# Performance work log

Hardware: AMD Instinct MI355X
Metric: run time of the kernel (lower is better)

## Reference

```python
import jax, jax.numpy as jnp
import numpy as np
import math

B, S, D, H, TD = 256, 200, 64, 512, 8


def setup_inputs():
    key = jax.random.key(0)
    ks = jax.random.split(key, 12)
    sd, sh, so = 1.0 / math.sqrt(D), 1.0 / math.sqrt(H), 1.0 / math.sqrt(H + TD)
    return dict(
        x=jax.random.normal(ks[0], (B, S, D), jnp.float32),
        a=jax.random.normal(ks[3], (B, TD), jnp.float32),
        t=jnp.cumsum(jax.random.uniform(ks[2], (B, S), jnp.float32), axis=1),
        mask=(jax.random.uniform(ks[1], (B, S, D)) < 0.8).astype(jnp.float32),
        w_dg_x=jax.random.normal(ks[4], (D,), jnp.float32) * sd,
        b_dg_x=jnp.zeros((D,), jnp.float32),
        W_dg_h=jax.random.normal(ks[5], (H, D), jnp.float32) * sd,
        b_dg_h=jnp.zeros((H,), jnp.float32),
        W=jax.random.normal(ks[6], (3 * H, D), jnp.float32) * sd,
        U=jax.random.normal(ks[7], (3 * H, H), jnp.float32) * sh,
        V=jax.random.normal(ks[8], (3 * H, D), jnp.float32) * sd,
        b=jnp.zeros((3 * H,), jnp.float32),
        attn_v=jnp.ones((H,), jnp.float32),
        W_out=jax.random.normal(ks[9], (H, H + TD), jnp.float32) * so,
        b_out=jnp.zeros((H,), jnp.float32),
    )


def reference(x, a, t, mask, w_dg_x, b_dg_x, W_dg_h, b_dg_h, W, U, V, b, attn_v, W_out, b_out):
    # ---- GRU-D preprocessing: per-feature time gaps delta ----
    x_tm = jnp.transpose(x, (1, 0, 2))    # (S,B,D) time-major
    m_tm = jnp.transpose(mask, (1, 0, 2))
    dt = jnp.diff(t, axis=1, prepend=t[:, :1])      # (B,S), dt[0]=0
    dt_tm = jnp.transpose(dt)[:, :, None]           # (S,B,1)
    # delta[i] = dt[i] + (1 - mask[i-1]) * delta[i-1]; ones at step 0 -> delta[0]=0
    m_prev = jnp.concatenate([jnp.ones((1,) + m_tm.shape[1:], m_tm.dtype), m_tm[:-1]], axis=0)

    def delta_step(d, inp):
        dt_i, mp_i = inp
        d = dt_i + (1.0 - mp_i) * d
        return d, d

    _, delta_tm = jax.lax.scan(delta_step, jnp.zeros((B, D), x.dtype), (dt_tm, m_prev))

    # empirical mean of observed values for imputation
    x_mean = (mask * x).sum((0, 1)) / jnp.maximum(mask.sum((0, 1)), 1.0)  # (D,)

    Wz, Wr, Wh = W[:H], W[H:2 * H], W[2 * H:]
    Uz, Ur, Uh = U[:H], U[H:2 * H], U[2 * H:]
    Vz, Vr, Vh = V[:H], V[H:2 * H], V[2 * H:]
    bz, br, bh = b[:H], b[H:2 * H], b[2 * H:]

    def cell(carry, inp):
        h, x_last = carry
        x_i, m_i, d_i = inp                                        # (B,D) each
        gamma_x = jnp.exp(-jax.nn.relu(w_dg_x * d_i + b_dg_x))     # (B,D) input decay
        gamma_h = jnp.exp(-jax.nn.relu(d_i @ W_dg_h.T + b_dg_h))   # (B,H) hidden decay
        x_hat = m_i * x_i + (1.0 - m_i) * (gamma_x * x_last + (1.0 - gamma_x) * x_mean)
        h_dec = gamma_h * h
        z = jax.nn.sigmoid(x_hat @ Wz.T + h_dec @ Uz.T + m_i @ Vz.T + bz)
        r = jax.nn.sigmoid(x_hat @ Wr.T + h_dec @ Ur.T + m_i @ Vr.T + br)
        h_til = jnp.tanh(x_hat @ Wh.T + (r * h_dec) @ Uh.T + m_i @ Vh.T + bh)
        h_new = (1.0 - z) * h_dec + z * h_til
        x_last_new = m_i * x_i + (1.0 - m_i) * x_last
        return (h_new, x_last_new), h_new

    init = (jnp.zeros((B, H), x.dtype), jnp.zeros((B, D), x.dtype))
    _, h_all = jax.lax.scan(cell, init, (x_tm, m_tm, delta_tm))    # (S,B,H)

    # ---- attention pooling over time (softmax along seq dim, as in torch dim=0) ----
    score = (h_all @ attn_v) / math.sqrt(H)        # (S,B)
    w_attn = jax.nn.softmax(score, axis=0)
    attn_h = (h_all * w_attn[..., None]).sum(0)    # (B,H)

    # ---- treatment head ----
    return jnp.concatenate([attn_h, a], axis=1) @ W_out.T + b_out  # (B,H)
```

## Files before the change

### kernel.cpp

```cpp
#include <hip/hip_runtime.h>
#include <hip/hip_bf16.h>
#include <stdint.h>


typedef unsigned short u16;
typedef unsigned int   u32;
typedef unsigned long long u64;
typedef short bfrag  __attribute__((ext_vector_type(8)));
typedef u16   u16x8  __attribute__((ext_vector_type(8)));
typedef float f32x4  __attribute__((ext_vector_type(4)));

#define NB 256
#define NS 200
#define ND 64
#define NH 512

union UQ  { u16x8 h; bfrag s; u64 u[2]; uint4 q; };
union UF2 { float f[2]; u64 u; };

__device__ __forceinline__ float b2f(u16 v){ union { float f; u32 u; } c; c.u = ((u32)v) << 16; return c.f; }
__device__ __forceinline__ u16 f2b(float f){ union { float f; u32 u; } c; c.f = f; u32 r = c.u + 0x7FFFu + ((c.u >> 16) & 1u); return (u16)(r >> 16); }
__device__ __forceinline__ float sigm(float x){ return 1.f / (1.f + __expf(-x)); }
__device__ __forceinline__ float tanh_f(float x){ return 1.f - 2.f / (1.f + __expf(2.f * x)); }

__device__ __forceinline__ u64 cload64(const void* p){
  return __hip_atomic_load((const u64*)p, __ATOMIC_RELAXED, __HIP_MEMORY_SCOPE_AGENT);
}
__device__ __forceinline__ void cstore64(void* p, u64 v){
  __hip_atomic_store((u64*)p, v, __ATOMIC_RELAXED, __HIP_MEMORY_SCOPE_AGENT);
}
__device__ __forceinline__ void load8f_c(const float* p, float* f){
  UF2 w;
  w.u = cload64(p + 0); f[0]=w.f[0]; f[1]=w.f[1];
  w.u = cload64(p + 2); f[2]=w.f[0]; f[3]=w.f[1];
  w.u = cload64(p + 4); f[4]=w.f[0]; f[5]=w.f[1];
  w.u = cload64(p + 6); f[6]=w.f[0]; f[7]=w.f[1];
}
__device__ __forceinline__ void store8f_c(float* p, const float* f){
  UF2 w;
  w.f[0]=f[0]; w.f[1]=f[1]; cstore64(p + 0, w.u);
  w.f[0]=f[2]; w.f[1]=f[3]; cstore64(p + 2, w.u);
  w.f[0]=f[4]; w.f[1]=f[5]; cstore64(p + 4, w.u);
  w.f[0]=f[6]; w.f[1]=f[7]; cstore64(p + 6, w.u);
}
__device__ __forceinline__ void spin_ge(u32* f, u32 tgt){
  while (__hip_atomic_load(f, __ATOMIC_RELAXED, __HIP_MEMORY_SCOPE_AGENT) < tgt)
    __builtin_amdgcn_s_sleep(2);
}
__device__ __forceinline__ bfrag ldfrag(const float* src){
  f32x4 lo = *(const f32x4*)src;
  f32x4 hi = *(const f32x4*)(src + 4);
  UQ z;
  z.h[0]=f2b(lo[0]); z.h[1]=f2b(lo[1]); z.h[2]=f2b(lo[2]); z.h[3]=f2b(lo[3]);
  z.h[4]=f2b(hi[0]); z.h[5]=f2b(hi[1]); z.h[6]=f2b(hi[2]); z.h[7]=f2b(hi[3]);
  return z.s;
}


__global__ void transpose_k(const float* __restrict__ Wout, float* __restrict__ WT){
  int i = blockIdx.x * 256 + threadIdx.x;
  if (i < 520 * 512) { int k = i >> 9, ho = i & 511; WT[i] = Wout[ho * 520 + k]; }
}

__global__ void mean1_k(const float* __restrict__ x, const float* __restrict__ mask,
                        float* __restrict__ PX, float* __restrict__ PM){
  int s = blockIdx.x, tid = threadIdx.x;
  __shared__ float lx[256], lm[256];
  float xa = 0.f, ma = 0.f;
  for (int i = tid; i < NB * ND; i += 256) {
    int b = i >> 6, d = i & 63;
    size_t ix = ((size_t)b * NS + s) * 64 + d;
    float m = mask[ix];
    xa += m * x[ix]; ma += m;
  }
  lx[tid] = xa; lm[tid] = ma;
  __syncthreads();
  if (tid < 64) {
    PX[(size_t)s * 64 + tid] = lx[tid] + lx[tid + 64] + lx[tid + 128] + lx[tid + 192];
    PM[(size_t)s * 64 + tid] = lm[tid] + lm[tid + 64] + lm[tid + 128] + lm[tid + 192];
  }
}

__global__ void mean2_k(const float* __restrict__ PX, const float* __restrict__ PM,
                        float* __restrict__ XMEAN){
  int d = threadIdx.x;
  float sx = 0.f, sm = 0.f;
  for (int s = 0; s < NS; ++s){ sx += PX[s * 64 + d]; sm += PM[s * 64 + d]; }
  XMEAN[d] = sx / fmaxf(sm, 1.f);
}

__global__ void prep_k(const float* __restrict__ x, const float* __restrict__ mask,
                       const float* __restrict__ tc, const float* __restrict__ wdgx,
                       const float* __restrict__ bdgx, const float* __restrict__ XMEAN,
                       u16* __restrict__ XHAT, u16* __restrict__ MASKB, u16* __restrict__ DELTA){
  int g = blockIdx.x * 256 + threadIdx.x;
  int b = g >> 6, d = g & 63;
  float xmean = XMEAN[d], wx = wdgx[d], bx = bdgx[d];
  float xl = 0.f, del = 0.f, tprev = 0.f, mprev = 1.f;
  for (int s = 0; s < NS; ++s){
    float tv = tc[b * NS + s];
    float dtv = (s == 0) ? 0.f : (tv - tprev);
    tprev = tv;
    del = dtv + (1.f - mprev) * del;
    size_t ix = ((size_t)b * NS + s) * 64 + d;
    float m = mask[ix], xv = x[ix];
    float gx = __expf(-fmaxf(0.f, wx * del + bx));
    float xh = m * xv + (1.f - m) * (gx * xl + (1.f - gx) * xmean);
    size_t ox = ((size_t)s * NB + b) * 64 + d;
    XHAT[ox] = f2b(xh); MASKB[ox] = f2b(m); DELTA[ox] = f2b(del);
    xl = m * xv + (1.f - m) * xl;
    mprev = m;
  }
}

__global__ __launch_bounds__(256, 1) void grud_rnn(
    const float* __restrict__ Um, const float* __restrict__ Wm, const float* __restrict__ Vm,
    const float* __restrict__ bv, const float* __restrict__ Wdg, const float* __restrict__ bdg,
    const u16* __restrict__ XHAT, const u16* __restrict__ MASKB, const u16* __restrict__ DELTA,
    float* __restrict__ HDEC, u16* __restrict__ RHD, float* __restrict__ ZB,
    float* __restrict__ SHP, u16* __restrict__ HALL, u32* done1, u32* done2)
{
  const int tid = threadIdx.x, lane = tid & 63, wid = tid >> 6, bid = blockIdx.x;
  __shared__ u16 panel[80 * 16 * 8];
  __shared__ u16 dpanel[8 * 16 * 8];
  __shared__ float xpose[4][528];
  float* xp = xpose[wid];
  const int r = lane >> 2, cb = (lane & 3) * 8;
  const int krow = lane >> 4;

  if (bid < 192) {
    const int rb = bid / 12, sg = bid % 12;
    const int type = (sg < 4) ? 0 : ((sg < 8) ? 1 : 2);
    const int st = sg * 4 + wid;
    const int cglob = st * 32;
    const int m0 = rb * 16;
    const int c0 = cglob + (lane & 15);

    bfrag Bf[20][2];
    #pragma unroll
    for (int kk = 0; kk < 20; ++kk) {
      if (!(type == 2 && kk < 16)) {
        const int k0 = kk * 32 + krow * 8;
        #pragma unroll
        for (int t2 = 0; t2 < 2; ++t2) {
          const int c = c0 + t2 * 16;
          const float* src;
          if (k0 < 512)      src = Um + (size_t)c * 512 + k0;
          else if (k0 < 576) src = Wm + (size_t)c * 64 + (k0 - 512);
          else               src = Vm + (size_t)c * 64 + (k0 - 576);
          Bf[kk][t2] = ldfrag(src);
        }
      }
    }
    const float bias0 = bv[c0], bias1 = bv[c0 + 16];

    for (int t = 0; t < NS; ++t) {
      {
        const int isrc = tid >> 7, row = (tid >> 3) & 15, kb8 = tid & 7;
        const u16* sp = (isrc ? MASKB : XHAT) + ((size_t)t * NB + (m0 + row)) * 64 + kb8 * 8;
        uint4 vv = *(const uint4*)sp;
        *(uint4*)&panel[(((isrc ? 72 : 64) + kb8) * 16 + row) * 8] = vv;
      }
      if (tid == 0) spin_ge(done2 + rb * 16, 4u * (u32)t);
      __syncthreads();
      if (type != 2) {
        #pragma unroll
        for (int it = 0; it < 4; ++it) {
          const int c = it * 256 + tid;
          const int row = c >> 6, kb = c & 63;
          float f[8];
          load8f_c(HDEC + (size_t)(m0 + row) * 512 + kb * 8, f);
          UQ pv;
          #pragma unroll
          for (int j = 0; j < 8; ++j) pv.h[j] = f2b(f[j]);
          *(u16x8*)&panel[(kb * 16 + row) * 8] = pv.h;
        }
      }
      __syncthreads();
      f32x4 acc0 = {bias0, bias0, bias0, bias0};
      f32x4 acc1 = {bias1, bias1, bias1, bias1};
      #pragma unroll
      for (int kk = 0; kk < 20; ++kk) {
        if (!(type == 2 && kk < 16)) {
          bfrag a = *(const bfrag*)&panel[((kk * 4 + krow) * 16 + (lane & 15)) * 8];
          acc0 = __builtin_amdgcn_mfma_f32_16x16x32_bf16(a, Bf[kk][0], acc0, 0, 0, 0);
          acc1 = __builtin_amdgcn_mfma_f32_16x16x32_bf16(a, Bf[kk][1], acc1, 0, 0, 0);
        }
      }
      {
        const int r0 = krow * 4, cc = lane & 15;
        #pragma unroll
        for (int j = 0; j < 4; ++j) { xp[(r0 + j) * 33 + cc] = acc0[j]; xp[(r0 + j) * 33 + 16 + cc] = acc1[j]; }
      }
      float s8[8];
      #pragma unroll
      for (int q = 0; q < 8; ++q) s8[q] = xp[r * 33 + cb + q];
      const size_t orow = (size_t)(m0 + r) * 512;
      if (type == 0) {
        float zf[8];
        #pragma unroll
        for (int q = 0; q < 8; ++q) zf[q] = sigm(s8[q]);
        store8f_c(ZB + orow + cglob + cb, zf);
      } else if (type == 1) {
        const int hc = cglob - 512 + cb;
        UQ hv; hv.h = *(const u16x8*)&panel[((hc >> 3) * 16 + r) * 8];
        UQ pv;
        #pragma unroll
        for (int q = 0; q < 8; ++q) pv.h[q] = f2b(sigm(s8[q]) * b2f(hv.h[q]));
        u16* dst = RHD + orow + hc;
        cstore64(dst, pv.u[0]); cstore64(dst + 4, pv.u[1]);
      } else {
        store8f_c(SHP + orow + (cglob - 1024) + cb, s8);
      }
      asm volatile("s_waitcnt vmcnt(0)" ::: "memory");
      __syncthreads();
      if (tid == 0) __hip_atomic_fetch_add(done1 + rb * 16, 1u, __ATOMIC_RELAXED, __HIP_MEMORY_SCOPE_AGENT);
    }
  } else {
    const int b2 = bid - 192;
    const int rb = b2 >> 2, sg = b2 & 3;
    const int st = sg * 4 + wid;
    const int n0 = st * 32;
    const int m0 = rb * 16;
    const int c0 = n0 + (lane & 15);

    bfrag Bh[16][2];
    #pragma unroll
    for (int kk = 0; kk < 16; ++kk) {
      const int k0 = kk * 32 + krow * 8;
      #pragma unroll
      for (int t2 = 0; t2 < 2; ++t2)
        Bh[kk][t2] = ldfrag(Um + (size_t)(1024 + c0 + t2 * 16) * 512 + k0);
    }
    bfrag Bg[2][2];
    #pragma unroll
    for (int kk = 0; kk < 2; ++kk) {
      const int k0 = kk * 32 + krow * 8;
      #pragma unroll
      for (int t2 = 0; t2 < 2; ++t2)
        Bg[kk][t2] = ldfrag(Wdg + (size_t)(c0 + t2 * 16) * 64 + k0);
    }
    const float gb0 = bdg[c0], gb1 = bdg[c0 + 16];

    for (int t = 0; t < NS; ++t) {
      float gam[8] = {0,0,0,0,0,0,0,0};
      if (t < NS - 1) {
        if (tid < 128) {
          const int row = (tid >> 3) & 15, kb8 = tid & 7;
          const u16* sp = DELTA + ((size_t)(t + 1) * NB + (m0 + row)) * 64 + kb8 * 8;
          *(uint4*)&dpanel[(kb8 * 16 + row) * 8] = *(const uint4*)sp;
        }
        __syncthreads();
        f32x4 g0 = {gb0, gb0, gb0, gb0};
        f32x4 g1 = {gb1, gb1, gb1, gb1};
        #pragma unroll
        for (int kk = 0; kk < 2; ++kk) {
          bfrag a = *(const bfrag*)&dpanel[((kk * 4 + krow) * 16 + (lane & 15)) * 8];
          g0 = __builtin_amdgcn_mfma_f32_16x16x32_bf16(a, Bg[kk][0], g0, 0, 0, 0);
          g1 = __builtin_amdgcn_mfma_f32_16x16x32_bf16(a, Bg[kk][1], g1, 0, 0, 0);
        }
        const int r0 = krow * 4, cc = lane & 15;
        #pragma unroll
        for (int j = 0; j < 4; ++j) { xp[(r0 + j) * 33 + cc] = g0[j]; xp[(r0 + j) * 33 + 16 + cc] = g1[j]; }
        #pragma unroll
        for (int q = 0; q < 8; ++q) gam[q] = __expf(-fmaxf(0.f, xp[r * 33 + cb + q]));
      }
      if (tid == 0) spin_ge(done1 + rb * 16, 12u * (u32)(t + 1));
      __syncthreads();
      #pragma unroll
      for (int it = 0; it < 4; ++it) {
        const int c = it * 256 + tid;
        const int row = c >> 6, kb = c & 63;
        const u16* sp = RHD + (size_t)(m0 + row) * 512 + kb * 8;
        UQ pv; pv.u[0] = cload64(sp); pv.u[1] = cload64(sp + 4);
        *(u16x8*)&panel[(kb * 16 + row) * 8] = pv.h;
      }
      __syncthreads();
      f32x4 acc0 = {0.f, 0.f, 0.f, 0.f}, acc1 = {0.f, 0.f, 0.f, 0.f};
      #pragma unroll
      for (int kk = 0; kk < 16; ++kk) {
        bfrag a = *(const bfrag*)&panel[((kk * 4 + krow) * 16 + (lane & 15)) * 8];
        acc0 = __builtin_amdgcn_mfma_f32_16x16x32_bf16(a, Bh[kk][0], acc0, 0, 0, 0);
        acc1 = __builtin_amdgcn_mfma_f32_16x16x32_bf16(a, Bh[kk][1], acc1, 0, 0, 0);
      }
      {
        const int r0 = krow * 4, cc = lane & 15;
        #pragma unroll
        for (int j = 0; j < 4; ++j) { xp[(r0 + j) * 33 + cc] = acc0[j]; xp[(r0 + j) * 33 + 16 + cc] = acc1[j]; }
      }
      const int hc = n0 + cb;
      const size_t orow = (size_t)(m0 + r) * 512;
      float s2[8], shp[8], zz[8], hd[8], hn[8], hdn[8];
      #pragma unroll
      for (int q = 0; q < 8; ++q) s2[q] = xp[r * 33 + cb + q];
      load8f_c(SHP + orow + hc, shp);
      load8f_c(ZB + orow + hc, zz);
      load8f_c(HDEC + orow + hc, hd);
      UQ hw;
      #pragma unroll
      for (int q = 0; q < 8; ++q) {
        float til = tanh_f(shp[q] + s2[q]);
        hn[q] = (1.f - zz[q]) * hd[q] + zz[q] * til;
        hw.h[q] = f2b(hn[q]);
        hdn[q] = gam[q] * hn[q];
      }
      u16* hp = HALL + ((size_t)t * NB + (m0 + r)) * 512 + hc;
      cstore64(hp, hw.u[0]); cstore64(hp + 4, hw.u[1]);
      if (t < NS - 1) store8f_c(HDEC + orow + hc, hdn);
      asm volatile("s_waitcnt vmcnt(0)" ::: "memory");
      __syncthreads();
      if (tid == 0) __hip_atomic_fetch_add(done2 + rb * 16, 1u, __ATOMIC_RELAXED, __HIP_MEMORY_SCOPE_AGENT);
    }
  }
}


__global__ void attn_k(const u16* __restrict__ HALL, const float* __restrict__ av,
                       float* __restrict__ ATTN){
  const int b = blockIdx.x, tid = threadIdx.x, lane = tid & 63, wid = tid >> 6;
  __shared__ float avs[512], wgt[256], red[8];
  for (int i = tid; i < 512; i += 256) avs[i] = av[i];
  __syncthreads();
  float val = -3.0e38f;
  if (tid < NS) {
    const u16* hp = HALL + ((size_t)tid * NB + b) * 512;
    float acc = 0.f;
    for (int h = 0; h < 512; h += 8) {
      UQ w; w.q = *(const uint4*)(hp + h);
      #pragma unroll
      for (int j = 0; j < 8; ++j) acc += b2f(w.h[j]) * avs[h + j];
    }
    val = acc * 0.04419417382415922f;
  }
  float m = val;
  #pragma unroll
  for (int off = 32; off; off >>= 1) m = fmaxf(m, __shfl_xor(m, off, 64));
  if (lane == 0) red[wid] = m;
  __syncthreads();
  m = fmaxf(fmaxf(red[0], red[1]), fmaxf(red[2], red[3]));
  float e = (tid < NS) ? __expf(val - m) : 0.f;
  float sum = e;
  #pragma unroll
  for (int off = 32; off; off >>= 1) sum += __shfl_xor(sum, off, 64);
  if (lane == 0) red[4 + wid] = sum;
  __syncthreads();
  const float ssum = red[4] + red[5] + red[6] + red[7];
  wgt[tid] = e / ssum;
  __syncthreads();
  float a0 = 0.f, a1 = 0.f;
  const int h0 = tid * 2;
  for (int s = 0; s < NS; ++s) {
    float w = wgt[s];
    u32 pr = *(const u32*)(HALL + ((size_t)s * NB + b) * 512 + h0);
    a0 += w * b2f((u16)(pr & 0xFFFFu));
    a1 += w * b2f((u16)(pr >> 16));
  }
  ATTN[(size_t)b * 512 + h0] = a0;
  ATTN[(size_t)b * 512 + h0 + 1] = a1;
}

__global__ void out_k(const float* __restrict__ ATTN, const float* __restrict__ Ain,
                      const float* __restrict__ WT, const float* __restrict__ bout,
                      float* __restrict__ OUT){
  const int b = blockIdx.x, tid = threadIdx.x;
  __shared__ float ah[512], aa[8];
  for (int i = tid; i < 512; i += 256) ah[i] = ATTN[(size_t)b * 512 + i];
  if (tid < 8) aa[tid] = Ain[b * 8 + tid];
  __syncthreads();
  #pragma unroll
  for (int part = 0; part < 2; ++part) {
    const int ho = part * 256 + tid;
    float acc = bout[ho];
    #pragma unroll 8
    for (int k = 0; k < 512; ++k) acc += ah[k] * WT[(size_t)k * 512 + ho];
    #pragma unroll
    for (int k = 0; k < 8; ++k) acc += aa[k] * WT[(size_t)(512 + k) * 512 + ho];
    OUT[(size_t)b * 512 + ho] = acc;
  }
}


extern "C" void kernel_launch(void* const* d_in, const int* in_sizes, int n_in,
                              void* d_out, int out_size, void* d_ws, size_t ws_size,
                              hipStream_t stream) {
  (void)in_sizes; (void)n_in; (void)out_size; (void)ws_size;
  const float* x    = (const float*)d_in[0];
  const float* a_in = (const float*)d_in[1];
  const float* tc   = (const float*)d_in[2];
  const float* mask = (const float*)d_in[3];
  const float* wdgx = (const float*)d_in[4];
  const float* bdgx = (const float*)d_in[5];
  const float* Wdgh = (const float*)d_in[6];
  const float* bdgh = (const float*)d_in[7];
  const float* Wm   = (const float*)d_in[8];
  const float* Um   = (const float*)d_in[9];
  const float* Vm   = (const float*)d_in[10];
  const float* bvv  = (const float*)d_in[11];
  const float* attv = (const float*)d_in[12];
  const float* Wout = (const float*)d_in[13];
  const float* bout = (const float*)d_in[14];

  char* ws = (char*)d_ws;
  size_t o = 0;
  auto al = [&](size_t sz) { size_t r = o; o += (sz + 255) & ~(size_t)255; return r; };
  u32*   flags = (u32*)  (ws + al(4096));
  float* XMEAN = (float*)(ws + al(256));
  float* PX    = (float*)(ws + al((size_t)NS * 64 * 4));
  float* PM    = (float*)(ws + al((size_t)NS * 64 * 4));
  u16*   XHAT  = (u16*)  (ws + al((size_t)NS * NB * 64 * 2));
  u16*   MASKB = (u16*)  (ws + al((size_t)NS * NB * 64 * 2));
  u16*   DELTA = (u16*)  (ws + al((size_t)NS * NB * 64 * 2));
  float* HDEC  = (float*)(ws + al((size_t)NB * NH * 4));
  u16*   RHD   = (u16*)  (ws + al((size_t)NB * NH * 2));
  float* ZB    = (float*)(ws + al((size_t)NB * NH * 4));
  float* SHP   = (float*)(ws + al((size_t)NB * NH * 4));
  u16*   HALL  = (u16*)  (ws + al((size_t)NS * NB * NH * 2));
  float* ATTN  = (float*)(ws + al((size_t)NB * NH * 4));
  float* WT    = (float*)(ws + al((size_t)520 * 512 * 4));
  u32* done1 = flags;
  u32* done2 = flags + 256;

  hipMemsetAsync(flags, 0, 4096, stream);
  hipMemsetAsync(HDEC, 0, (size_t)NB * NH * 4, stream);

  transpose_k<<<(520 * 512 + 255) / 256, 256, 0, stream>>>(Wout, WT);
  mean1_k<<<NS, 256, 0, stream>>>(x, mask, PX, PM);
  mean2_k<<<1, 64, 0, stream>>>(PX, PM, XMEAN);
  prep_k<<<NB * ND / 256, 256, 0, stream>>>(x, mask, tc, wdgx, bdgx, XMEAN, XHAT, MASKB, DELTA);
  grud_rnn<<<256, 256, 0, stream>>>(Um, Wm, Vm, bvv, Wdgh, bdgh, XHAT, MASKB, DELTA,
                                    HDEC, RHD, ZB, SHP, HALL, done1, done2);
  attn_k<<<NB, 256, 0, stream>>>(HALL, attv, ATTN);
  out_k<<<NB, 256, 0, stream>>>(ATTN, a_in, WT, bout, (float*)d_out);
}
```

Baseline: 2.266 ms.

## Restructure GRU-D persistent kernel into specialized roles to shorten per-step critical path

Splits the persistent recurrent kernel into 15 roles per row block: z/r gate workgroups that also compute partial (r*h_dec)@Uh products, workgroups that precompute the input/mask part of the candidate gate one step ahead, a workgroup that precomputes hidden decay gamma, and elementwise workgroups that reduce the partials and update h. The decayed hidden state is now stored in bf16 and kept in registers by the updater, which removes one dependent GEMM stage and one global round-trip per timestep. Spin waits gain a timeout that aborts the loop, and the output head now processes four batch rows per block to reuse weight loads. In exchange there are more flag handshakes and partial-sum traffic, and if a timeout fires the result is silently wrong.

```diff
diff --git a/kernel.cpp b/kernel.cpp
--- a/kernel.cpp
+++ b/kernel.cpp
@@ -15,6 +15,8 @@
 #define ND 64
 #define NH 512
 
+#define MFMA(a,b,c) __builtin_amdgcn_mfma_f32_16x16x32_bf16((a),(b),(c),0,0,0)
+
 union UQ  { u16x8 h; bfrag s; u64 u[2]; uint4 q; };
 union UF2 { float f[2]; u64 u; };
 
@@ -43,9 +45,13 @@
   w.f[0]=f[4]; w.f[1]=f[5]; cstore64(p + 4, w.u);
   w.f[0]=f[6]; w.f[1]=f[7]; cstore64(p + 6, w.u);
 }
-__device__ __forceinline__ void spin_ge(u32* f, u32 tgt){
-  while (__hip_atomic_load(f, __ATOMIC_RELAXED, __HIP_MEMORY_SCOPE_AGENT) < tgt)
-    __builtin_amdgcn_s_sleep(2);
+__device__ __forceinline__ bool spin_ge(u32* f, u32 tgt){
+  int fuel = 1 << 19;
+  while (__hip_atomic_load(f, __ATOMIC_RELAXED, __HIP_MEMORY_SCOPE_AGENT) < tgt) {
+    __builtin_amdgcn_s_sleep(1);
+    if (--fuel == 0) return false;
+  }
+  return true;
 }
 __device__ __forceinline__ bfrag ldfrag(const float* src){
   f32x4 lo = *(const f32x4*)src;
@@ -117,199 +123,292 @@
     const float* __restrict__ Um, const float* __restrict__ Wm, const float* __restrict__ Vm,
     const float* __restrict__ bv, const float* __restrict__ Wdg, const float* __restrict__ bdg,
     const u16* __restrict__ XHAT, const u16* __restrict__ MASKB, const u16* __restrict__ DELTA,
-    float* __restrict__ HDEC, u16* __restrict__ RHD, float* __restrict__ ZB,
-    float* __restrict__ SHP, u16* __restrict__ HALL, u32* done1, u32* done2)
+    u16* __restrict__ HDEC, float* __restrict__ ZB, float* __restrict__ PART,
+    float* __restrict__ SHXP, float* __restrict__ GAM, u16* __restrict__ HALL,
+    u32* __restrict__ flags)
 {
   const int tid = threadIdx.x, lane = tid & 63, wid = tid >> 6, bid = blockIdx.x;
+  const int rb = bid / 15, role = bid % 15, m0 = rb * 16;
+  const int l16 = lane & 15, krow = lane >> 4, r4 = lane >> 2, cb = (lane & 3) * 8;
+  u32* dZR = flags + rb * 32;
+  u32* dSH = flags + 512 + rb * 32;
+  u32* dG  = flags + 1024 + rb * 32;
+  u32* d2  = flags + 1536 + rb * 32;
+
   __shared__ u16 panel[80 * 16 * 8];
-  __shared__ u16 dpanel[8 * 16 * 8];
-  __shared__ float xpose[4][528];
-  float* xp = xpose[wid];
-  const int r = lane >> 2, cb = (lane & 3) * 8;
-  const int krow = lane >> 4;
-
-  if (bid < 192) {
-    const int rb = bid / 12, sg = bid % 12;
-    const int type = (sg < 4) ? 0 : ((sg < 8) ? 1 : 2);
-    const int st = sg * 4 + wid;
-    const int cglob = st * 32;
-    const int m0 = rb * 16;
-    const int c0 = cglob + (lane & 15);
-
-    bfrag Bf[20][2];
+  __shared__ u16 rhbuf[16 * 136];
+  __shared__ float xb[4][16 * 136];
+  __shared__ int s_ab;
+  float* xw = xb[wid];
+  const f32x4 Z4 = {0.f, 0.f, 0.f, 0.f};
+  if (tid == 0) s_ab = 0;
+  __syncthreads();
+
+  if (role < 8) {
+    const bool isr = role >= 4;
+    const int g = role & 3;
+    const int rc = g * 128 + wid * 32;
+    const int gb = (isr ? 512 : 0) + rc;
+
+    bfrag BU[16][2], BX[2][2], BM[2][2];
     #pragma unroll
-    for (int kk = 0; kk < 20; ++kk) {
-      if (!(type == 2 && kk < 16)) {
-        const int k0 = kk * 32 + krow * 8;
-        #pragma unroll
-        for (int t2 = 0; t2 < 2; ++t2) {
-          const int c = c0 + t2 * 16;
-          const float* src;
-          if (k0 < 512)      src = Um + (size_t)c * 512 + k0;
-          else if (k0 < 576) src = Wm + (size_t)c * 64 + (k0 - 512);
-          else               src = Vm + (size_t)c * 64 + (k0 - 576);
-          Bf[kk][t2] = ldfrag(src);
-        }
-      }
-    }
-    const float bias0 = bv[c0], bias1 = bv[c0 + 16];
+    for (int kk = 0; kk < 16; ++kk)
+      #pragma unroll
+      for (int t2 = 0; t2 < 2; ++t2)
+        BU[kk][t2] = ldfrag(Um + (size_t)(gb + t2 * 16 + l16) * 512 + kk * 32 + krow * 8);
+    #pragma unroll
+    for (int kx = 0; kx < 2; ++kx)
+      #pragma unroll
+      for (int t2 = 0; t2 < 2; ++t2) {
+        BX[kx][t2] = ldfrag(Wm + (size_t)(gb + t2 * 16 + l16) * 64 + kx * 32 + krow * 8);
+        BM[kx][t2] = ldfrag(Vm + (size_t)(gb + t2 * 16 + l16) * 64 + kx * 32 + krow * 8);
+      }
+    bfrag BH[4][8];
+    if (isr) {
+      #pragma unroll
+      for (int kf = 0; kf < 4; ++kf)
+        #pragma unroll
+        for (int nt = 0; nt < 8; ++nt)
+          BH[kf][nt] = ldfrag(Um + (size_t)(1024 + (wid * 8 + nt) * 16 + l16) * 512
+                              + g * 128 + kf * 32 + krow * 8);
+    }
+    const float bias0 = bv[gb + l16], bias1 = bv[gb + 16 + l16];
 
     for (int t = 0; t < NS; ++t) {
       {
-        const int isrc = tid >> 7, row = (tid >> 3) & 15, kb8 = tid & 7;
-        const u16* sp = (isrc ? MASKB : XHAT) + ((size_t)t * NB + (m0 + row)) * 64 + kb8 * 8;
-        uint4 vv = *(const uint4*)sp;
-        *(uint4*)&panel[(((isrc ? 72 : 64) + kb8) * 16 + row) * 8] = vv;
-      }
-      if (tid == 0) spin_ge(done2 + rb * 16, 4u * (u32)t);
-      __syncthreads();
-      if (type != 2) {
-        #pragma unroll
-        for (int it = 0; it < 4; ++it) {
-          const int c = it * 256 + tid;
-          const int row = c >> 6, kb = c & 63;
-          float f[8];
-          load8f_c(HDEC + (size_t)(m0 + row) * 512 + kb * 8, f);
-          UQ pv;
-          #pragma unroll
-          for (int j = 0; j < 8; ++j) pv.h[j] = f2b(f[j]);
-          *(u16x8*)&panel[(kb * 16 + row) * 8] = pv.h;
-        }
+        const int kbx = tid >> 4, row = tid & 15;
+        const u16* sp = (kbx < 8 ? XHAT : MASKB) + ((size_t)t * NB + m0 + row) * 64 + (kbx & 7) * 8;
+        *(uint4*)&panel[((64 + kbx) * 16 + row) * 8] = *(const uint4*)sp;
       }
       __syncthreads();
       f32x4 acc0 = {bias0, bias0, bias0, bias0};
       f32x4 acc1 = {bias1, bias1, bias1, bias1};
       #pragma unroll
-      for (int kk = 0; kk < 20; ++kk) {
-        if (!(type == 2 && kk < 16)) {
-          bfrag a = *(const bfrag*)&panel[((kk * 4 + krow) * 16 + (lane & 15)) * 8];
-          acc0 = __builtin_amdgcn_mfma_f32_16x16x32_bf16(a, Bf[kk][0], acc0, 0, 0, 0);
-          acc1 = __builtin_amdgcn_mfma_f32_16x16x32_bf16(a, Bf[kk][1], acc1, 0, 0, 0);
+      for (int kx = 0; kx < 2; ++kx) {
+        bfrag ax = *(const bfrag*)&panel[((64 + kx * 4 + krow) * 16 + l16) * 8];
+        acc0 = MFMA(ax, BX[kx][0], acc0); acc1 = MFMA(ax, BX[kx][1], acc1);
+        bfrag am = *(const bfrag*)&panel[((72 + kx * 4 + krow) * 16 + l16) * 8];
+        acc0 = MFMA(am, BM[kx][0], acc0); acc1 = MFMA(am, BM[kx][1], acc1);
+      }
+      if (tid == 0) { if (!spin_ge(d2, 4u * (u32)t)) s_ab = 1; }
+      __syncthreads();
+      if (s_ab) break;
+      #pragma unroll
+      for (int i = 0; i < 4; ++i) {
+        const int off = tid * 64 + i * 16;
+        const int row = off >> 10, kb = (off & 1023) >> 4;
+        const u16* sp = HDEC + (size_t)(m0 + row) * 512 + kb * 8;
+        u64 a = cload64(sp), b = cload64(sp + 4);
+        u16* dp = &panel[(kb * 16 + row) * 8];
+        *(u64*)dp = a; *(u64*)(dp + 4) = b;
+      }
+      __syncthreads();
+      #pragma unroll
+      for (int kk = 0; kk < 16; ++kk) {
+        bfrag a = *(const bfrag*)&panel[((kk * 4 + krow) * 16 + l16) * 8];
+        acc0 = MFMA(a, BU[kk][0], acc0); acc1 = MFMA(a, BU[kk][1], acc1);
+      }
+      #pragma unroll
+      for (int j = 0; j < 4; ++j) {
+        xw[(krow * 4 + j) * 136 + l16] = acc0[j];
+        xw[(krow * 4 + j) * 136 + 16 + l16] = acc1[j];
+      }
+      float s8[8];
+      #pragma unroll
+      for (int q = 0; q < 8; ++q) s8[q] = xw[r4 * 136 + cb + q];
+      if (!isr) {
+        float zf[8];
+        #pragma unroll
+        for (int q = 0; q < 8; ++q) zf[q] = sigm(s8[q]);
+        store8f_c(ZB + (size_t)(m0 + r4) * 512 + rc + cb, zf);
+      } else {
+        UQ hv; hv.h = *(const u16x8*)&panel[(((rc + cb) >> 3) * 16 + r4) * 8];
+        UQ pv;
+        #pragma unroll
+        for (int q = 0; q < 8; ++q) pv.h[q] = f2b(sigm(s8[q]) * b2f(hv.h[q]));
+        *(u16x8*)&rhbuf[r4 * 136 + wid * 32 + cb] = pv.h;
+        __syncthreads();
+        bfrag af[4];
+        #pragma unroll
+        for (int kf = 0; kf < 4; ++kf)
+          af[kf] = *(const bfrag*)&rhbuf[l16 * 136 + kf * 32 + krow * 8];
+        f32x4 sacc[8];
+        #pragma unroll
+        for (int nt = 0; nt < 8; ++nt) {
+          f32x4 s = Z4;
+          #pragma unroll
+          for (int kf = 0; kf < 4; ++kf) s = MFMA(af[kf], BH[kf][nt], s);
+          sacc[nt] = s;
         }
-      }
-      {
-        const int r0 = krow * 4, cc = lane & 15;
-        #pragma unroll
-        for (int j = 0; j < 4; ++j) { xp[(r0 + j) * 33 + cc] = acc0[j]; xp[(r0 + j) * 33 + 16 + cc] = acc1[j]; }
-      }
-      float s8[8];
-      #pragma unroll
-      for (int q = 0; q < 8; ++q) s8[q] = xp[r * 33 + cb + q];
-      const size_t orow = (size_t)(m0 + r) * 512;
-      if (type == 0) {
-        float zf[8];
-        #pragma unroll
-        for (int q = 0; q < 8; ++q) zf[q] = sigm(s8[q]);
-        store8f_c(ZB + orow + cglob + cb, zf);
-      } else if (type == 1) {
-        const int hc = cglob - 512 + cb;
-        UQ hv; hv.h = *(const u16x8*)&panel[((hc >> 3) * 16 + r) * 8];
-        UQ pv;
-        #pragma unroll
-        for (int q = 0; q < 8; ++q) pv.h[q] = f2b(sigm(s8[q]) * b2f(hv.h[q]));
-        u16* dst = RHD + orow + hc;
-        cstore64(dst, pv.u[0]); cstore64(dst + 4, pv.u[1]);
-      } else {
-        store8f_c(SHP + orow + (cglob - 1024) + cb, s8);
+        #pragma unroll
+        for (int nt = 0; nt < 8; ++nt)
+          #pragma unroll
+          for (int j = 0; j < 4; ++j)
+            xw[(krow * 4 + j) * 136 + nt * 16 + l16] = sacc[nt][j];
+        float* dst = PART + (size_t)(rb * 4 + g) * 8192 + (size_t)r4 * 512
+                     + wid * 128 + (lane & 3) * 32;
+        #pragma unroll
+        for (int c = 0; c < 8; ++c) {
+          f32x4 v = *(const f32x4*)&xw[r4 * 136 + (lane & 3) * 32 + c * 4];
+          UF2 w0; w0.f[0] = v[0]; w0.f[1] = v[1]; cstore64(dst + c * 4, w0.u);
+          UF2 w1; w1.f[0] = v[2]; w1.f[1] = v[3]; cstore64(dst + c * 4 + 2, w1.u);
+        }
       }
       asm volatile("s_waitcnt vmcnt(0)" ::: "memory");
       __syncthreads();
-      if (tid == 0) __hip_atomic_fetch_add(done1 + rb * 16, 1u, __ATOMIC_RELAXED, __HIP_MEMORY_SCOPE_AGENT);
+      if (tid == 0) __hip_atomic_fetch_add(dZR, 1u, __ATOMIC_RELAXED, __HIP_MEMORY_SCOPE_AGENT);
+    }
+  } else if (role < 10) {
+    const int shwg = role - 8;
+    const int hbase = (shwg * 4 + wid) * 64;
+    bfrag BS[4][4];
+    #pragma unroll
+    for (int kx = 0; kx < 4; ++kx)
+      #pragma unroll
+      for (int ct = 0; ct < 4; ++ct)
+        BS[kx][ct] = (kx < 2)
+          ? ldfrag(Wm + (size_t)(1024 + hbase + ct * 16 + l16) * 64 + kx * 32 + krow * 8)
+          : ldfrag(Vm + (size_t)(1024 + hbase + ct * 16 + l16) * 64 + (kx - 2) * 32 + krow * 8);
+    float bb[4];
+    #pragma unroll
+    for (int ct = 0; ct < 4; ++ct) bb[ct] = bv[1024 + hbase + ct * 16 + l16];
+
+    for (int t = 0; t < NS; ++t) {
+      { const int kbx = tid >> 4, row = tid & 15;
+        const u16* sp = (kbx < 8 ? XHAT : MASKB) + ((size_t)t * NB + m0 + row) * 64 + (kbx & 7) * 8;
+        *(uint4*)&panel[(kbx * 16 + row) * 8] = *(const uint4*)sp; }
+      __syncthreads();
+      f32x4 acc[4];
+      #pragma unroll
+      for (int ct = 0; ct < 4; ++ct) acc[ct] = (f32x4){bb[ct], bb[ct], bb[ct], bb[ct]};
+      #pragma unroll
+      for (int kx = 0; kx < 4; ++kx) {
+        const int pk = (kx < 2) ? (kx * 4 + krow) : (8 + (kx - 2) * 4 + krow);
+        bfrag a = *(const bfrag*)&panel[(pk * 16 + l16) * 8];
+        #pragma unroll
+        for (int ct = 0; ct < 4; ++ct) acc[ct] = MFMA(a, BS[kx][ct], acc[ct]);
+      }
+      #pragma unroll
+      for (int ct = 0; ct < 4; ++ct)
+        #pragma unroll
+        for (int j = 0; j < 4; ++j)
+          xw[(krow * 4 + j) * 136 + ct * 16 + l16] = acc[ct][j];
+      float out[16];
+      #pragma unroll
+      for (int c = 0; c < 4; ++c) {
+        f32x4 v = *(const f32x4*)&xw[r4 * 136 + (lane & 3) * 16 + c * 4];
+        out[c*4] = v[0]; out[c*4+1] = v[1]; out[c*4+2] = v[2]; out[c*4+3] = v[3];
+      }
+      if (tid == 0 && t >= 2) { if (!spin_ge(d2, 4u * (u32)(t - 1))) s_ab = 1; }
+      __syncthreads();
+      if (s_ab) break;
+      float* dst = SHXP + ((size_t)(t & 1) * 16 + rb) * 8192 + (size_t)r4 * 512
+                   + hbase + (lane & 3) * 16;
+      #pragma unroll
+      for (int c = 0; c < 8; ++c) {
+        UF2 w; w.f[0] = out[c*2]; w.f[1] = out[c*2+1]; cstore64(dst + c * 2, w.u);
+      }
+      asm volatile("s_waitcnt vmcnt(0)" ::: "memory");
+      __syncthreads();
+      if (tid == 0) __hip_atomic_fetch_add(dSH, 1u, __ATOMIC_RELAXED, __HIP_MEMORY_SCOPE_AGENT);
+    }
+  } else if (role == 10) {
+    bfrag BG[2][8];
+    #pragma unroll
+    for (int kx = 0; kx < 2; ++kx)
+      #pragma unroll
+      for (int ct = 0; ct < 8; ++ct)
+        BG[kx][ct] = ldfrag(Wdg + (size_t)(wid * 128 + ct * 16 + l16) * 64 + kx * 32 + krow * 8);
+    float gbias[8];
+    #pragma unroll
+    for (int ct = 0; ct < 8; ++ct) gbias[ct] = bdg[wid * 128 + ct * 16 + l16];
+
+    for (int g2 = 1; g2 < NS; ++g2) {
+      if (tid < 128) {
+        const int kbx = tid >> 4, row = tid & 15;
+        const u16* sp = DELTA + ((size_t)g2 * NB + m0 + row) * 64 + kbx * 8;
+        *(uint4*)&panel[(kbx * 16 + row) * 8] = *(const uint4*)sp;
+      }
+      __syncthreads();
+      f32x4 acc[8];
+      #pragma unroll
+      for (int ct = 0; ct < 8; ++ct) acc[ct] = (f32x4){gbias[ct], gbias[ct], gbias[ct], gbias[ct]};
+      #pragma unroll
+      for (int kx = 0; kx < 2; ++kx) {
+        bfrag a = *(const bfrag*)&panel[((kx * 4 + krow) * 16 + l16) * 8];
+        #pragma unroll
+        for (int ct = 0; ct < 8; ++ct) acc[ct] = MFMA(a, BG[kx][ct], acc[ct]);
+      }
+      #pragma unroll
+      for (int ct = 0; ct < 8; ++ct)
+        #pragma unroll
+        for (int j = 0; j < 4; ++j)
+          xw[(krow * 4 + j) * 136 + ct * 16 + l16] = acc[ct][j];
+      float gm[32];
+      #pragma unroll
+      for (int c = 0; c < 8; ++c) {
+        f32x4 v = *(const f32x4*)&xw[r4 * 136 + (lane & 3) * 32 + c * 4];
+        gm[c*4]   = __expf(-fmaxf(0.f, v[0]));
+        gm[c*4+1] = __expf(-fmaxf(0.f, v[1]));
+        gm[c*4+2] = __expf(-fmaxf(0.f, v[2]));
+        gm[c*4+3] = __expf(-fmaxf(0.f, v[3]));
+      }
+      if (tid == 0 && g2 >= 3) { if (!spin_ge(d2, 4u * (u32)(g2 - 2))) s_ab = 1; }
+      __syncthreads();
+      if (s_ab) break;
+      float* dst = GAM + ((size_t)(g2 & 1) * 16 + rb) * 8192 + (size_t)r4 * 512 + wid * 128 + (lane & 3) * 32;
+      #pragma unroll
+      for (int c = 0; c < 16; ++c) {
+        UF2 w; w.f[0] = gm[c*2]; w.f[1] = gm[c*2+1]; cstore64(dst + c * 2, w.u);
+      }
+      asm volatile("s_waitcnt vmcnt(0)" ::: "memory");
+      __syncthreads();
+      if (tid == 0) __hip_atomic_fetch_add(dG, 1u, __ATOMIC_RELAXED, __HIP_MEMORY_SCOPE_AGENT);
     }
   } else {
-    const int b2 = bid - 192;
-    const int rb = b2 >> 2, sg = b2 & 3;
-    const int st = sg * 4 + wid;
-    const int n0 = st * 32;
-    const int m0 = rb * 16;
-    const int c0 = n0 + (lane & 15);
-
-    bfrag Bh[16][2];
-    #pragma unroll
-    for (int kk = 0; kk < 16; ++kk) {
-      const int k0 = kk * 32 + krow * 8;
-      #pragma unroll
-      for (int t2 = 0; t2 < 2; ++t2)
-        Bh[kk][t2] = ldfrag(Um + (size_t)(1024 + c0 + t2 * 16) * 512 + k0);
-    }
-    bfrag Bg[2][2];
-    #pragma unroll
-    for (int kk = 0; kk < 2; ++kk) {
-      const int k0 = kk * 32 + krow * 8;
-      #pragma unroll
-      for (int t2 = 0; t2 < 2; ++t2)
-        Bg[kk][t2] = ldfrag(Wdg + (size_t)(c0 + t2 * 16) * 64 + k0);
-    }
-    const float gb0 = bdg[c0], gb1 = bdg[c0 + 16];
+    const int ewg = role - 11;
+    const int n0 = (ewg * 4 + wid) * 32;
+    float hd[8] = {0.f,0.f,0.f,0.f,0.f,0.f,0.f,0.f};
+    const size_t rowoff = (size_t)r4 * 512 + n0 + cb;
 
     for (int t = 0; t < NS; ++t) {
-      float gam[8] = {0,0,0,0,0,0,0,0};
-      if (t < NS - 1) {
-        if (tid < 128) {
-          const int row = (tid >> 3) & 15, kb8 = tid & 7;
-          const u16* sp = DELTA + ((size_t)(t + 1) * NB + (m0 + row)) * 64 + kb8 * 8;
-          *(uint4*)&dpanel[(kb8 * 16 + row) * 8] = *(const uint4*)sp;
-        }
-        __syncthreads();
-        f32x4 g0 = {gb0, gb0, gb0, gb0};
-        f32x4 g1 = {gb1, gb1, gb1, gb1};
-        #pragma unroll
-        for (int kk = 0; kk < 2; ++kk) {
-          bfrag a = *(const bfrag*)&dpanel[((kk * 4 + krow) * 16 + (lane & 15)) * 8];
-          g0 = __builtin_amdgcn_mfma_f32_16x16x32_bf16(a, Bg[kk][0], g0, 0, 0, 0);
-          g1 = __builtin_amdgcn_mfma_f32_16x16x32_bf16(a, Bg[kk][1], g1, 0, 0, 0);
-        }
-        const int r0 = krow * 4, cc = lane & 15;
-        #pragma unroll
-        for (int j = 0; j < 4; ++j) { xp[(r0 + j) * 33 + cc] = g0[j]; xp[(r0 + j) * 33 + 16 + cc] = g1[j]; }
-        #pragma unroll
-        for (int q = 0; q < 8; ++q) gam[q] = __expf(-fmaxf(0.f, xp[r * 33 + cb + q]));
-      }
-      if (tid == 0) spin_ge(done1 + rb * 16, 12u * (u32)(t + 1));
-      __syncthreads();
-      #pragma unroll
-      for (int it = 0; it < 4; ++it) {
-        const int c = it * 256 + tid;
-        const int row = c >> 6, kb = c & 63;
-        const u16* sp = RHD + (size_t)(m0 + row) * 512 + kb * 8;
-        UQ pv; pv.u[0] = cload64(sp); pv.u[1] = cload64(sp + 4);
-        *(u16x8*)&panel[(kb * 16 + row) * 8] = pv.h;
-      }
-      __syncthreads();
-      f32x4 acc0 = {0.f, 0.f, 0.f, 0.f}, acc1 = {0.f, 0.f, 0.f, 0.f};
-      #pragma unroll
-      for (int kk = 0; kk < 16; ++kk) {
-        bfrag a = *(const bfrag*)&panel[((kk * 4 + krow) * 16 + (lane & 15)) * 8];
-        acc0 = __builtin_amdgcn_mfma_f32_16x16x32_bf16(a, Bh[kk][0], acc0, 0, 0, 0);
-        acc1 = __builtin_amdgcn_mfma_f32_16x16x32_bf16(a, Bh[kk][1], acc1, 0, 0, 0);
-      }
-      {
-        const int r0 = krow * 4, cc = lane & 15;
-        #pragma unroll
-        for (int j = 0; j < 4; ++j) { xp[(r0 + j) * 33 + cc] = acc0[j]; xp[(r0 + j) * 33 + 16 + cc] = acc1[j]; }
-      }
-      const int hc = n0 + cb;
-      const size_t orow = (size_t)(m0 + r) * 512;
-      float s2[8], shp[8], zz[8], hd[8], hn[8], hdn[8];
-      #pragma unroll
-      for (int q = 0; q < 8; ++q) s2[q] = xp[r * 33 + cb + q];
-      load8f_c(SHP + orow + hc, shp);
-      load8f_c(ZB + orow + hc, zz);
-      load8f_c(HDEC + orow + hc, hd);
+      if (tid == 64) { if (!spin_ge(dSH, 2u * (u32)(t + 1))) s_ab = 1; }
+      if (tid == 128 && t < NS - 1) { if (!spin_ge(dG, (u32)(t + 1))) s_ab = 1; }
+      __syncthreads();
+      if (s_ab) break;
+      float shx[8], gm[8];
+      load8f_c(SHXP + ((size_t)(t & 1) * 16 + rb) * 8192 + rowoff, shx);
+      if (t < NS - 1)
+        load8f_c(GAM + ((size_t)((t + 1) & 1) * 16 + rb) * 8192 + rowoff, gm);
+      if (tid == 0) { if (!spin_ge(dZR, 8u * (u32)(t + 1))) s_ab = 1; }
+      __syncthreads();
+      if (s_ab) break;
+      float p0[8], p1[8], p2[8], p3[8], zz[8];
+      load8f_c(PART + (size_t)(rb * 4 + 0) * 8192 + rowoff, p0);
+      load8f_c(PART + (size_t)(rb * 4 + 1) * 8192 + rowoff, p1);
+      load8f_c(PART + (size_t)(rb * 4 + 2) * 8192 + rowoff, p2);
+      load8f_c(PART + (size_t)(rb * 4 + 3) * 8192 + rowoff, p3);
+      load8f_c(ZB + (size_t)(m0 + r4) * 512 + n0 + cb, zz);
       UQ hw;
+      float hn[8];
       #pragma unroll
       for (int q = 0; q < 8; ++q) {
-        float til = tanh_f(shp[q] + s2[q]);
+        float til = tanh_f(shx[q] + p0[q] + p1[q] + p2[q] + p3[q]);
         hn[q] = (1.f - zz[q]) * hd[q] + zz[q] * til;
         hw.h[q] = f2b(hn[q]);
-        hdn[q] = gam[q] * hn[q];
-      }
-      u16* hp = HALL + ((size_t)t * NB + (m0 + r)) * 512 + hc;
+      }
+      if (t < NS - 1) {
+        UQ hv;
+        #pragma unroll
+        for (int q = 0; q < 8; ++q) { hd[q] = gm[q] * hn[q]; hv.h[q] = f2b(hd[q]); }
+        u16* dp = HDEC + (size_t)(m0 + r4) * 512 + n0 + cb;
+        cstore64(dp, hv.u[0]); cstore64(dp + 4, hv.u[1]);
+      }
+      asm volatile("s_waitcnt vmcnt(0)" ::: "memory");
+      __syncthreads();
+      if (tid == 0) __hip_atomic_fetch_add(d2, 1u, __ATOMIC_RELAXED, __HIP_MEMORY_SCOPE_AGENT);
+      u16* hp = HALL + ((size_t)t * NB + m0 + r4) * 512 + n0 + cb;
       cstore64(hp, hw.u[0]); cstore64(hp + 4, hw.u[1]);
-      if (t < NS - 1) store8f_c(HDEC + orow + hc, hdn);
-      asm volatile("s_waitcnt vmcnt(0)" ::: "memory");
-      __syncthreads();
-      if (tid == 0) __hip_atomic_fetch_add(done2 + rb * 16, 1u, __ATOMIC_RELAXED, __HIP_MEMORY_SCOPE_AGENT);
     }
   }
 }
@@ -362,20 +461,26 @@
 __global__ void out_k(const float* __restrict__ ATTN, const float* __restrict__ Ain,
                       const float* __restrict__ WT, const float* __restrict__ bout,
                       float* __restrict__ OUT){
-  const int b = blockIdx.x, tid = threadIdx.x;
-  __shared__ float ah[512], aa[8];
-  for (int i = tid; i < 512; i += 256) ah[i] = ATTN[(size_t)b * 512 + i];
-  if (tid < 8) aa[tid] = Ain[b * 8 + tid];
+  const int g = blockIdx.x, tid = threadIdx.x;
+  __shared__ float ah[4][520];
+  for (int i = tid; i < 4 * 520; i += 256) {
+    int bb = i / 520, k = i % 520;
+    int b = g * 4 + bb;
+    ah[bb][k] = (k < 512) ? ATTN[(size_t)b * 512 + k] : Ain[b * 8 + (k - 512)];
+  }
   __syncthreads();
   #pragma unroll
   for (int part = 0; part < 2; ++part) {
     const int ho = part * 256 + tid;
-    float acc = bout[ho];
-    #pragma unroll 8
-    for (int k = 0; k < 512; ++k) acc += ah[k] * WT[(size_t)k * 512 + ho];
-    #pragma unroll
-    for (int k = 0; k < 8; ++k) acc += aa[k] * WT[(size_t)(512 + k) * 512 + ho];
-    OUT[(size_t)b * 512 + ho] = acc;
+    float a0 = bout[ho], a1 = a0, a2 = a0, a3 = a0;
+    for (int k = 0; k < 520; ++k) {
+      float w = WT[(size_t)k * 512 + ho];
+      a0 += ah[0][k] * w; a1 += ah[1][k] * w; a2 += ah[2][k] * w; a3 += ah[3][k] * w;
+    }
+    OUT[(size_t)(g * 4 + 0) * 512 + ho] = a0;
+    OUT[(size_t)(g * 4 + 1) * 512 + ho] = a1;
+    OUT[(size_t)(g * 4 + 2) * 512 + ho] = a2;
+    OUT[(size_t)(g * 4 + 3) * 512 + ho] = a3;
   }
 }
 
@@ -403,32 +508,31 @@
   char* ws = (char*)d_ws;
   size_t o = 0;
   auto al = [&](size_t sz) { size_t r = o; o += (sz + 255) & ~(size_t)255; return r; };
-  u32*   flags = (u32*)  (ws + al(4096));
+  u32*   flags = (u32*)  (ws + al(8192));
   float* XMEAN = (float*)(ws + al(256));
   float* PX    = (float*)(ws + al((size_t)NS * 64 * 4));
   float* PM    = (float*)(ws + al((size_t)NS * 64 * 4));
   u16*   XHAT  = (u16*)  (ws + al((size_t)NS * NB * 64 * 2));
   u16*   MASKB = (u16*)  (ws + al((size_t)NS * NB * 64 * 2));
   u16*   DELTA = (u16*)  (ws + al((size_t)NS * NB * 64 * 2));
-  float* HDEC  = (float*)(ws + al((size_t)NB * NH * 4));
-  u16*   RHD   = (u16*)  (ws + al((size_t)NB * NH * 2));
+  u16*   HDEC  = (u16*)  (ws + al((size_t)NB * NH * 2));
   float* ZB    = (float*)(ws + al((size_t)NB * NH * 4));
-  float* SHP   = (float*)(ws + al((size_t)NB * NH * 4));
+  float* PARTB = (float*)(ws + al((size_t)16 * 4 * 8192 * 4));
+  float* SHXP  = (float*)(ws + al((size_t)2 * 16 * 8192 * 4));
+  float* GAM   = (float*)(ws + al((size_t)2 * 16 * 8192 * 4));
   u16*   HALL  = (u16*)  (ws + al((size_t)NS * NB * NH * 2));
   float* ATTN  = (float*)(ws + al((size_t)NB * NH * 4));
   float* WT    = (float*)(ws + al((size_t)520 * 512 * 4));
-  u32* done1 = flags;
-  u32* done2 = flags + 256;
-
-  hipMemsetAsync(flags, 0, 4096, stream);
-  hipMemsetAsync(HDEC, 0, (size_t)NB * NH * 4, stream);
+
+  hipMemsetAsync(flags, 0, 8192, stream);
+  hipMemsetAsync(HDEC, 0, (size_t)NB * NH * 2, stream);
 
   transpose_k<<<(520 * 512 + 255) / 256, 256, 0, stream>>>(Wout, WT);
   mean1_k<<<NS, 256, 0, stream>>>(x, mask, PX, PM);
   mean2_k<<<1, 64, 0, stream>>>(PX, PM, XMEAN);
   prep_k<<<NB * ND / 256, 256, 0, stream>>>(x, mask, tc, wdgx, bdgx, XMEAN, XHAT, MASKB, DELTA);
-  grud_rnn<<<256, 256, 0, stream>>>(Um, Wm, Vm, bvv, Wdgh, bdgh, XHAT, MASKB, DELTA,
-                                    HDEC, RHD, ZB, SHP, HALL, done1, done2);
+  grud_rnn<<<240, 256, 0, stream>>>(Um, Wm, Vm, bvv, Wdgh, bdgh, XHAT, MASKB, DELTA,
+                                    HDEC, ZB, PARTB, SHXP, GAM, HALL, flags);
   attn_k<<<NB, 256, 0, stream>>>(HALL, attv, ATTN);
-  out_k<<<NB, 256, 0, stream>>>(ATTN, a_in, WT, bout, (float*)d_out);
-}
+  out_k<<<64, 256, 0, stream>>>(ATTN, a_in, WT, bout, (float*)d_out);
+}
```

New measurement: 3.188 ms. +40.7%, slower.
